# Kernel optimization log

Hardware: AMD Instinct MI355X
Metric: run time of the kernel (lower is better)

Reference implementation:

```python
import jax, jax.numpy as jnp
import numpy as np

N = 50000        # nodes
E = 800000       # directed edges (before self-loops)
F_IN = 128       # num_features
GAT_DIM = 16     # per-head channels
HEADS = 4
HID = GAT_DIM * HEADS   # 64, concat output of each GATConv
FC = 10 * GAT_DIM       # 160
OUT = 64                # output_dim
NEG_SLOPE = 0.2         # PyG GATConv default


def _gat_conv(x, W, a_src, a_dst, b, src, dst):
    """One PyG-style GATConv (concat=True, self-loops already in src/dst).
    x: [N, Fin], W: [Fin, HEADS*GAT_DIM], a_src/a_dst: [HEADS, GAT_DIM], b: [HEADS*GAT_DIM]."""
    H, C = a_src.shape
    h = (x @ W).reshape(N, H, C)                       # [N,H,C]
    s_src = (h * a_src).sum(-1)                        # [N,H] per-node src score
    s_dst = (h * a_dst).sum(-1)                        # [N,H]
    e = jax.nn.leaky_relu(s_src[src] + s_dst[dst], NEG_SLOPE)  # [Etot,H]
    # segment softmax over incoming edges of each destination node
    m = jax.ops.segment_max(e, dst, num_segments=N)    # [N,H]
    ex = jnp.exp(e - m[dst])
    z = jax.ops.segment_sum(ex, dst, num_segments=N)   # [N,H]
    alpha = ex / (z[dst] + 1e-16)                      # [Etot,H]
    msg = h[src] * alpha[:, :, None]                   # [Etot,H,C]
    out = jax.ops.segment_sum(msg, dst, num_segments=N)
    return out.reshape(N, H * C) + b


def setup_inputs() -> dict:
    key = jax.random.key(0)
    ks = jax.random.split(key, 20)
    sc = 0.05
    inp = {
        "x": jax.random.normal(ks[0], (N, F_IN), dtype=jnp.float32),
        "edge_index": jax.random.randint(ks[1], (2, E), 0, N, dtype=jnp.int32),
        "W0": jax.random.normal(ks[2], (F_IN, HID), dtype=jnp.float32) * sc,
        "as0": jax.random.normal(ks[3], (HEADS, GAT_DIM), dtype=jnp.float32) * sc,
        "ad0": jax.random.normal(ks[4], (HEADS, GAT_DIM), dtype=jnp.float32) * sc,
        "b0": jnp.zeros((HID,), jnp.float32),
        "W1": jax.random.normal(ks[5], (HID, HID), dtype=jnp.float32) * sc,
        "as1": jax.random.normal(ks[6], (HEADS, GAT_DIM), dtype=jnp.float32) * sc,
        "ad1": jax.random.normal(ks[7], (HEADS, GAT_DIM), dtype=jnp.float32) * sc,
        "b1": jnp.zeros((HID,), jnp.float32),
        "W2": jax.random.normal(ks[8], (HID, HID), dtype=jnp.float32) * sc,
        "as2": jax.random.normal(ks[9], (HEADS, GAT_DIM), dtype=jnp.float32) * sc,
        "ad2": jax.random.normal(ks[10], (HEADS, GAT_DIM), dtype=jnp.float32) * sc,
        "b2": jnp.zeros((HID,), jnp.float32),
        "fw1": jax.random.normal(ks[11], (HID, FC), dtype=jnp.float32) * sc,
        "fb1": jnp.zeros((FC,), jnp.float32),
        "fw2": jax.random.normal(ks[12], (FC, OUT), dtype=jnp.float32) * sc,
        "fb2": jnp.zeros((OUT,), jnp.float32),
    }
    return inp


def reference(x, edge_index, W0, as0, ad0, b0, W1, as1, ad1, b1, W2, as2, ad2, b2, fw1, fb1, fw2, fb2):
    loop = jnp.arange(N, dtype=edge_index.dtype)
    src = jnp.concatenate([edge_index[0], loop])   # PyG add_self_loops=True
    dst = jnp.concatenate([edge_index[1], loop])
    h = jax.nn.relu(_gat_conv(x, W0, as0, ad0, b0, src, dst))
    h = jax.nn.relu(_gat_conv(h, W1, as1, ad1, b1, src, dst))
    h = jax.nn.relu(_gat_conv(h, W2, as2, ad2, b2, src, dst))
    h = jax.nn.relu(h @ fw1 + fb1)
    return h @ fw2 + fb2
```

## Files before the change

### kernel.cpp

```cpp
#include <hip/hip_runtime.h>
#include <hip/hip_fp16.h>

#define NN 50000
#define EE 800000
#define ETOT (EE + NN)
#define HIDD 64
#define NHEADS 4
#define FCD 160
#define OUTD 64

#define NBKT 196
#define BSTRIDE 5120
#define CHUNK 4096
#define NEBLK ((ETOT + CHUNK - 1) / CHUNK)
#define NGB   ((NN + 63) / 64)
#define NFC128 ((NN + 127) / 128)


__global__ void k_zero(int* __restrict__ cursor) {
    int t = threadIdx.x;
    if (t < NBKT) cursor[t] = 0;
}

__global__ __launch_bounds__(256) void k_binwrite(const int* __restrict__ ei,
                                                  int* __restrict__ cursor,
                                                  unsigned* __restrict__ binned) {
    __shared__ int hist[NBKT];
    __shared__ int sbase[NBKT];
    __shared__ int cur[NBKT];
    int t = threadIdx.x;
    for (int i = t; i < NBKT; i += 256) hist[i] = 0;
    __syncthreads();
    int base = blockIdx.x * CHUNK;
    for (int k = t; k < CHUNK; k += 256) {
        int i = base + k;
        if (i < ETOT) {
            int dst = (i < EE) ? ei[EE + i] : (i - EE);
            atomicAdd(&hist[dst >> 8], 1);
        }
    }
    __syncthreads();
    for (int b = t; b < NBKT; b += 256) {
        int c = hist[b];
        sbase[b] = b * BSTRIDE + (c ? atomicAdd(&cursor[b], c) : 0);
        cur[b] = 0;
    }
    __syncthreads();
    for (int k = t; k < CHUNK; k += 256) {
        int i = base + k;
        if (i < ETOT) {
            int src, dst;
            if (i < EE) { src = ei[i]; dst = ei[EE + i]; }
            else { src = dst = i - EE; }
            int b = dst >> 8;
            int p = atomicAdd(&cur[b], 1);
            binned[sbase[b] + p] = ((unsigned)src << 8) | (unsigned)(dst & 255);
        }
    }
}

__global__ __launch_bounds__(256) void k_csr_final(const int* __restrict__ cursor,
                                                   const unsigned* __restrict__ binned,
                                                   int* __restrict__ rowbeg,
                                                   int* __restrict__ rowend,
                                                   int* __restrict__ csrc) {
    __shared__ int hist[256];
    __shared__ int cur[256];
    __shared__ int wsum[4];
    int b = blockIdx.x;
    int t = threadIdx.x;
    int s0 = b * BSTRIDE;
    int cnt = cursor[b];
    hist[t] = 0;
    __syncthreads();
    for (int k = t; k < cnt; k += 256) {
        unsigned pr = binned[s0 + k];
        atomicAdd(&hist[pr & 255u], 1);
    }
    __syncthreads();
    int v = hist[t];
    int lane = t & 63, w = t >> 6;
    int x = v;
    #pragma unroll
    for (int off = 1; off < 64; off <<= 1) {
        int y = __shfl_up(x, off);
        if (lane >= off) x += y;
    }
    if (lane == 63) wsum[w] = x;
    __syncthreads();
    int add = 0;
    #pragma unroll
    for (int k = 0; k < 4; k++) add += (k < w) ? wsum[k] : 0;
    int excl = x + add - v;
    int n = (b << 8) + t;
    if (n < NN) {
        rowbeg[n] = s0 + excl;
        rowend[n] = s0 + excl + v;
    }
    cur[t] = s0 + excl;
    __syncthreads();
    for (int k = t; k < cnt; k += 256) {
        unsigned pr = binned[s0 + k];
        int p = atomicAdd(&cur[pr & 255u], 1);
        csrc[p] = (int)(pr >> 8);
    }
}


template<int FIN>
__global__ __launch_bounds__(256) void k_gemm_scores(
        const float* __restrict__ x, const float* __restrict__ W,
        const float* __restrict__ a_src, const float* __restrict__ a_dst,
        __half* __restrict__ h, float* __restrict__ ssrc, float* __restrict__ sdst) {
    __shared__ float wl[64 * 64];
    __shared__ float xt[64][68];
    int t = threadIdx.x;
    int nb = blockIdx.x * 64;
    int qg = t & 15, ng = t >> 4;
    float acc[4][4] = {};
    const float4* wl4 = (const float4*)wl;

    #pragma unroll
    for (int p = 0; p < FIN / 64; p++) {
        if (p) __syncthreads();
        for (int i = t; i < 64 * 64 / 4; i += 256)
            ((float4*)wl)[i] = ((const float4*)W)[p * 1024 + i];
        #pragma unroll
        for (int r = 0; r < 4; r++) {
            int idx = t + r * 256;
            int node = idx & 63, kq = idx >> 6;
            int n = nb + node;
            float4 v = make_float4(0.f, 0.f, 0.f, 0.f);
            if (n < NN) v = *(const float4*)(x + (size_t)n * FIN + p * 64 + kq * 4);
            xt[kq * 4 + 0][node] = v.x;
            xt[kq * 4 + 1][node] = v.y;
            xt[kq * 4 + 2][node] = v.z;
            xt[kq * 4 + 3][node] = v.w;
        }
        __syncthreads();
        #pragma unroll 4
        for (int k = 0; k < 64; k++) {
            float4 wv = wl4[k * 16 + qg];
            float4 xv = *(const float4*)&xt[k][ng * 4];
            acc[0][0] += xv.x * wv.x; acc[0][1] += xv.x * wv.y;
            acc[0][2] += xv.x * wv.z; acc[0][3] += xv.x * wv.w;
            acc[1][0] += xv.y * wv.x; acc[1][1] += xv.y * wv.y;
            acc[1][2] += xv.y * wv.z; acc[1][3] += xv.y * wv.w;
            acc[2][0] += xv.z * wv.x; acc[2][1] += xv.z * wv.y;
            acc[2][2] += xv.z * wv.z; acc[2][3] += xv.z * wv.w;
            acc[3][0] += xv.w * wv.x; acc[3][1] += xv.w * wv.y;
            acc[3][2] += xv.w * wv.z; acc[3][3] += xv.w * wv.w;
        }
    }

    #pragma unroll
    for (int r = 0; r < 4; r++) {
        int n = nb + ng * 4 + r;
        if (n < NN) {
            union { __half2 h2[2]; uint2 u; } pk;
            pk.h2[0] = __floats2half2_rn(acc[r][0], acc[r][1]);
            pk.h2[1] = __floats2half2_rn(acc[r][2], acc[r][3]);
            *(uint2*)(h + (size_t)n * HIDD + qg * 4) = pk.u;
        }
    }

    float as0 = a_src[qg * 4 + 0], as1 = a_src[qg * 4 + 1];
    float as2 = a_src[qg * 4 + 2], as3 = a_src[qg * 4 + 3];
    float ad0 = a_dst[qg * 4 + 0], ad1 = a_dst[qg * 4 + 1];
    float ad2 = a_dst[qg * 4 + 2], ad3 = a_dst[qg * 4 + 3];
    float vs[4], vd[4];
    #pragma unroll
    for (int r = 0; r < 4; r++) {
        vs[r] = acc[r][0] * as0 + acc[r][1] * as1 + acc[r][2] * as2 + acc[r][3] * as3;
        vd[r] = acc[r][0] * ad0 + acc[r][1] * ad1 + acc[r][2] * ad2 + acc[r][3] * ad3;
        vs[r] += __shfl_xor(vs[r], 1); vs[r] += __shfl_xor(vs[r], 2);
        vd[r] += __shfl_xor(vd[r], 1); vd[r] += __shfl_xor(vd[r], 2);
    }
    if ((qg & 3) == 0) {
        int hd = qg >> 2;
        #pragma unroll
        for (int r = 0; r < 4; r++) {
            int n = nb + ng * 4 + r;
            if (n < NN) {
                ssrc[n * NHEADS + hd] = vs[r];
                sdst[n * NHEADS + hd] = vd[r];
            }
        }
    }
}


__global__ __launch_bounds__(512) void k_aggr_gemm(
        const __half* __restrict__ h, const float* __restrict__ ssrc,
        const float* __restrict__ sdst, const int* __restrict__ rowbeg,
        const int* __restrict__ rowend, const int* __restrict__ csrc,
        const float* __restrict__ bias, const float* __restrict__ W,
        const float* __restrict__ a_src, const float* __restrict__ a_dst,
        __half* __restrict__ hout, float* __restrict__ ssrc_o,
        float* __restrict__ sdst_o) {
    __shared__ float wl[64 * 64];
    __shared__ float xt[64][68];
    int t = threadIdx.x;
    int nb = blockIdx.x * 64;

    for (int i = t; i < 64 * 64 / 4; i += 512)
        ((float4*)wl)[i] = ((const float4*)W)[i];

    {
        int wid = t >> 6, lane = t & 63;
        int sub = lane >> 4, c4 = lane & 15, hd = c4 >> 2;
        #pragma unroll 1
        for (int i = 0; i < 8; i++) {
            int nl = wid * 8 + i;
            int n = nb + nl;
            float4 acc = make_float4(0.f, 0.f, 0.f, 0.f);
            float z = 0.f;
            if (n < NN) {
                int beg = rowbeg[n], end = rowend[n];
                float sdh = sdst[n * NHEADS + hd];
                for (int cb = beg; cb < end; cb += 16) {
                    #pragma unroll
                    for (int o = 0; o < 4; o++) {
                        int e = cb + sub + o * 4;
                        if (e < end) {
                            int s = csrc[e];
                            float eh = ssrc[s * NHEADS + hd] + sdh;
                            eh = eh > 0.f ? eh : 0.2f * eh;
                            float w = __expf(eh);
                            uint2 r = *(const uint2*)(h + (size_t)s * HIDD + c4 * 4);
                            float2 lo = __half22float2(*(__half2*)&r.x);
                            float2 hi = __half22float2(*(__half2*)&r.y);
                            acc.x += lo.x * w; acc.y += lo.y * w;
                            acc.z += hi.x * w; acc.w += hi.y * w;
                            z += w;
                        }
                    }
                }
            }
            acc.x += __shfl_xor(acc.x, 16); acc.y += __shfl_xor(acc.y, 16);
            acc.z += __shfl_xor(acc.z, 16); acc.w += __shfl_xor(acc.w, 16);
            z += __shfl_xor(z, 16);
            acc.x += __shfl_xor(acc.x, 32); acc.y += __shfl_xor(acc.y, 32);
            acc.z += __shfl_xor(acc.z, 32); acc.w += __shfl_xor(acc.w, 32);
            z += __shfl_xor(z, 32);
            if (sub == 0) {
                float inv_z = 1.0f / (z + 1e-16f);
                float4 bv = *(const float4*)(bias + c4 * 4);
                float v0 = acc.x * inv_z + bv.x; v0 = v0 > 0.f ? v0 : 0.f;
                float v1 = acc.y * inv_z + bv.y; v1 = v1 > 0.f ? v1 : 0.f;
                float v2 = acc.z * inv_z + bv.z; v2 = v2 > 0.f ? v2 : 0.f;
                float v3 = acc.w * inv_z + bv.w; v3 = v3 > 0.f ? v3 : 0.f;
                if (n >= NN) { v0 = v1 = v2 = v3 = 0.f; }
                xt[c4 * 4 + 0][nl] = v0;
                xt[c4 * 4 + 1][nl] = v1;
                xt[c4 * 4 + 2][nl] = v2;
                xt[c4 * 4 + 3][nl] = v3;
            }
        }
    }
    __syncthreads();

    {
        int qg = t & 15, ng = t >> 4;
        float acc[2][4] = {};
        const float4* wl4 = (const float4*)wl;
        #pragma unroll 4
        for (int k = 0; k < 64; k++) {
            float4 wv = wl4[k * 16 + qg];
            float2 xv = *(const float2*)&xt[k][ng * 2];
            acc[0][0] += xv.x * wv.x; acc[0][1] += xv.x * wv.y;
            acc[0][2] += xv.x * wv.z; acc[0][3] += xv.x * wv.w;
            acc[1][0] += xv.y * wv.x; acc[1][1] += xv.y * wv.y;
            acc[1][2] += xv.y * wv.z; acc[1][3] += xv.y * wv.w;
        }
        #pragma unroll
        for (int r = 0; r < 2; r++) {
            int n = nb + ng * 2 + r;
            if (n < NN) {
                union { __half2 h2[2]; uint2 u; } pk;
                pk.h2[0] = __floats2half2_rn(acc[r][0], acc[r][1]);
                pk.h2[1] = __floats2half2_rn(acc[r][2], acc[r][3]);
                *(uint2*)(hout + (size_t)n * HIDD + qg * 4) = pk.u;
            }
        }
        float as0 = a_src[qg * 4 + 0], as1 = a_src[qg * 4 + 1];
        float as2 = a_src[qg * 4 + 2], as3 = a_src[qg * 4 + 3];
        float ad0 = a_dst[qg * 4 + 0], ad1 = a_dst[qg * 4 + 1];
        float ad2 = a_dst[qg * 4 + 2], ad3 = a_dst[qg * 4 + 3];
        float vs[2], vd[2];
        #pragma unroll
        for (int r = 0; r < 2; r++) {
            vs[r] = acc[r][0] * as0 + acc[r][1] * as1 + acc[r][2] * as2 + acc[r][3] * as3;
            vd[r] = acc[r][0] * ad0 + acc[r][1] * ad1 + acc[r][2] * ad2 + acc[r][3] * ad3;
            vs[r] += __shfl_xor(vs[r], 1); vs[r] += __shfl_xor(vs[r], 2);
            vd[r] += __shfl_xor(vd[r], 1); vd[r] += __shfl_xor(vd[r], 2);
        }
        if ((qg & 3) == 0) {
            int hd = qg >> 2;
            #pragma unroll
            for (int r = 0; r < 2; r++) {
                int n = nb + ng * 2 + r;
                if (n < NN) {
                    ssrc_o[n * NHEADS + hd] = vs[r];
                    sdst_o[n * NHEADS + hd] = vd[r];
                }
            }
        }
    }
}


__global__ __launch_bounds__(256) void k_aggr(
        const __half* __restrict__ h, const float* __restrict__ ssrc,
        const float* __restrict__ sdst, const int* __restrict__ rowbeg,
        const int* __restrict__ rowend,
        const int* __restrict__ csrc, const float* __restrict__ bias,
        float* __restrict__ out) {
    int wid  = threadIdx.x >> 6;
    int lane = threadIdx.x & 63;
    int n = blockIdx.x * 4 + wid;
    int sub = lane >> 4;
    int c4  = lane & 15;
    int hd  = c4 >> 2;
    int beg = rowbeg[n], end = rowend[n];
    float sdh = sdst[n * NHEADS + hd];

    float4 acc = make_float4(0.f, 0.f, 0.f, 0.f);
    float z = 0.f;
    for (int cb = beg; cb < end; cb += 16) {
        #pragma unroll
        for (int o = 0; o < 4; o++) {
            int e = cb + sub + o * 4;
            if (e < end) {
                int s = csrc[e];
                float eh = ssrc[s * NHEADS + hd] + sdh;
                eh = eh > 0.f ? eh : 0.2f * eh;
                float w = __expf(eh);
                uint2 r = *(const uint2*)(h + (size_t)s * HIDD + c4 * 4);
                float2 lo = __half22float2(*(__half2*)&r.x);
                float2 hi = __half22float2(*(__half2*)&r.y);
                acc.x += lo.x * w; acc.y += lo.y * w;
                acc.z += hi.x * w; acc.w += hi.y * w;
                z += w;
            }
        }
    }
    acc.x += __shfl_xor(acc.x, 16); acc.y += __shfl_xor(acc.y, 16);
    acc.z += __shfl_xor(acc.z, 16); acc.w += __shfl_xor(acc.w, 16);
    z += __shfl_xor(z, 16);
    acc.x += __shfl_xor(acc.x, 32); acc.y += __shfl_xor(acc.y, 32);
    acc.z += __shfl_xor(acc.z, 32); acc.w += __shfl_xor(acc.w, 32);
    z += __shfl_xor(z, 32);

    if (sub == 0) {
        float inv_z = 1.0f / (z + 1e-16f);
        float4 bv = *(const float4*)(bias + c4 * 4);
        float4 o;
        o.x = acc.x * inv_z + bv.x; o.x = o.x > 0.f ? o.x : 0.f;
        o.y = acc.y * inv_z + bv.y; o.y = o.y > 0.f ? o.y : 0.f;
        o.z = acc.z * inv_z + bv.z; o.z = o.z > 0.f ? o.z : 0.f;
        o.w = acc.w * inv_z + bv.w; o.w = o.w > 0.f ? o.w : 0.f;
        *(float4*)(out + (size_t)n * HIDD + c4 * 4) = o;
    }
}


__global__ __launch_bounds__(256) void k_fc_fused(const float* __restrict__ x,
        const float* __restrict__ W1, const float* __restrict__ b1,
        const float* __restrict__ W2, const float* __restrict__ b2,
        float* __restrict__ out) {
    __shared__ float wl[32 * 160];
    __shared__ float xt[32][132];
    __shared__ __half y[160][136];
    int t = threadIdx.x;
    int nb = blockIdx.x * 128;
    const float4* wl4 = (const float4*)wl;

    {
        int qg = t & 7, ng = t >> 3;
        float acc[4][5][4] = {};
        #pragma unroll
        for (int p = 0; p < 2; p++) {
            if (p) __syncthreads();
            for (int i = t; i < 32 * 160 / 4; i += 256)
                ((float4*)wl)[i] = ((const float4*)W1)[p * 32 * 40 + i];
            #pragma unroll
            for (int r = 0; r < 4; r++) {
                int idx = t + r * 256;
                int node = idx & 127, kq = idx >> 7;
                int n = nb + node;
                float4 v = make_float4(0.f, 0.f, 0.f, 0.f);
                if (n < NN) v = *(const float4*)(x + (size_t)n * 64 + p * 32 + kq * 4);
                xt[kq * 4 + 0][node] = v.x;
                xt[kq * 4 + 1][node] = v.y;
                xt[kq * 4 + 2][node] = v.z;
                xt[kq * 4 + 3][node] = v.w;
            }
            __syncthreads();
            #pragma unroll 4
            for (int k = 0; k < 32; k++) {
                float4 xv = *(const float4*)&xt[k][ng * 4];
                #pragma unroll
                for (int i = 0; i < 5; i++) {
                    float4 wv = wl4[k * 40 + qg + 8 * i];
                    acc[0][i][0] += xv.x * wv.x; acc[0][i][1] += xv.x * wv.y;
                    acc[0][i][2] += xv.x * wv.z; acc[0][i][3] += xv.x * wv.w;
                    acc[1][i][0] += xv.y * wv.x; acc[1][i][1] += xv.y * wv.y;
                    acc[1][i][2] += xv.y * wv.z; acc[1][i][3] += xv.y * wv.w;
                    acc[2][i][0] += xv.z * wv.x; acc[2][i][1] += xv.z * wv.y;
                    acc[2][i][2] += xv.z * wv.z; acc[2][i][3] += xv.z * wv.w;
                    acc[3][i][0] += xv.w * wv.x; acc[3][i][1] += xv.w * wv.y;
                    acc[3][i][2] += xv.w * wv.z; acc[3][i][3] += xv.w * wv.w;
                }
            }
        }
        #pragma unroll
        for (int i = 0; i < 5; i++) {
            int j0 = (qg + 8 * i) * 4;
            float4 bv = *(const float4*)(b1 + j0);
            #pragma unroll
            for (int r = 0; r < 4; r++) {
                int node = ng * 4 + r;
                float v0 = acc[r][i][0] + bv.x; v0 = v0 > 0.f ? v0 : 0.f;
                float v1 = acc[r][i][1] + bv.y; v1 = v1 > 0.f ? v1 : 0.f;
                float v2 = acc[r][i][2] + bv.z; v2 = v2 > 0.f ? v2 : 0.f;
                float v3 = acc[r][i][3] + bv.w; v3 = v3 > 0.f ? v3 : 0.f;
                y[j0 + 0][node] = __float2half_rn(v0);
                y[j0 + 1][node] = __float2half_rn(v1);
                y[j0 + 2][node] = __float2half_rn(v2);
                y[j0 + 3][node] = __float2half_rn(v3);
            }
        }
    }
    __syncthreads();

    {
        int qg = t & 15, ng = t >> 4;
        float acc[8][4] = {};
        #pragma unroll
        for (int p = 0; p < 2; p++) {
            if (p) __syncthreads();
            for (int i = t; i < 80 * 64 / 4; i += 256)
                ((float4*)wl)[i] = ((const float4*)W2)[p * 80 * 16 + i];
            __syncthreads();
            #pragma unroll 2
            for (int k = 0; k < 80; k++) {
                float4 wv = wl4[k * 16 + qg];
                uint4 yr = *(const uint4*)&y[p * 80 + k][ng * 8];
                float2 f0 = __half22float2(*(__half2*)&yr.x);
                float2 f1 = __half22float2(*(__half2*)&yr.y);
                float2 f2 = __half22float2(*(__half2*)&yr.z);
                float2 f3 = __half22float2(*(__half2*)&yr.w);
                acc[0][0] += f0.x * wv.x; acc[0][1] += f0.x * wv.y;
                acc[0][2] += f0.x * wv.z; acc[0][3] += f0.x * wv.w;
                acc[1][0] += f0.y * wv.x; acc[1][1] += f0.y * wv.y;
                acc[1][2] += f0.y * wv.z; acc[1][3] += f0.y * wv.w;
                acc[2][0] += f1.x * wv.x; acc[2][1] += f1.x * wv.y;
                acc[2][2] += f1.x * wv.z; acc[2][3] += f1.x * wv.w;
                acc[3][0] += f1.y * wv.x; acc[3][1] += f1.y * wv.y;
                acc[3][2] += f1.y * wv.z; acc[3][3] += f1.y * wv.w;
                acc[4][0] += f2.x * wv.x; acc[4][1] += f2.x * wv.y;
                acc[4][2] += f2.x * wv.z; acc[4][3] += f2.x * wv.w;
                acc[5][0] += f2.y * wv.x; acc[5][1] += f2.y * wv.y;
                acc[5][2] += f2.y * wv.z; acc[5][3] += f2.y * wv.w;
                acc[6][0] += f3.x * wv.x; acc[6][1] += f3.x * wv.y;
                acc[6][2] += f3.x * wv.z; acc[6][3] += f3.x * wv.w;
                acc[7][0] += f3.y * wv.x; acc[7][1] += f3.y * wv.y;
                acc[7][2] += f3.y * wv.z; acc[7][3] += f3.y * wv.w;
            }
        }
        int j0 = qg * 4;
        float4 bv = *(const float4*)(b2 + j0);
        #pragma unroll
        for (int r = 0; r < 8; r++) {
            int n = nb + ng * 8 + r;
            if (n < NN) {
                float4 o;
                o.x = acc[r][0] + bv.x; o.y = acc[r][1] + bv.y;
                o.z = acc[r][2] + bv.z; o.w = acc[r][3] + bv.w;
                *(float4*)(out + (size_t)n * 64 + j0) = o;
            }
        }
    }
}


extern "C" void kernel_launch(void* const* d_in, const int* in_sizes, int n_in,
                              void* d_out, int out_size, void* d_ws, size_t ws_size,
                              hipStream_t stream) {
    const float* x   = (const float*)d_in[0];
    const int*   ei  = (const int*)d_in[1];
    const float* W0  = (const float*)d_in[2];
    const float* as0 = (const float*)d_in[3];
    const float* ad0 = (const float*)d_in[4];
    const float* b0  = (const float*)d_in[5];
    const float* W1  = (const float*)d_in[6];
    const float* as1 = (const float*)d_in[7];
    const float* ad1 = (const float*)d_in[8];
    const float* b1  = (const float*)d_in[9];
    const float* W2  = (const float*)d_in[10];
    const float* as2 = (const float*)d_in[11];
    const float* ad2 = (const float*)d_in[12];
    const float* b2  = (const float*)d_in[13];
    const float* fw1 = (const float*)d_in[14];
    const float* fb1 = (const float*)d_in[15];
    const float* fw2 = (const float*)d_in[16];
    const float* fb2 = (const float*)d_in[17];

    float* ws = (float*)d_ws;
    __half* hA  = (__half*)ws;
    __half* hB  = (__half*)(ws + (size_t)NN * 32);
    float* sAsrc = ws + (size_t)NN * 64;
    float* sAdst = sAsrc + (size_t)NN * NHEADS;
    float* sBsrc = sAdst + (size_t)NN * NHEADS;
    float* sBdst = sBsrc + (size_t)NN * NHEADS;
    float* act   = sBdst + (size_t)NN * NHEADS;
    float* scr   = act + (size_t)NN * HIDD;
    unsigned* binned = (unsigned*)scr;
    int*   csrc   = (int*)scr + 1100000;
    int*   rowbeg = (int*)scr + 2200000;
    int*   rowend = (int*)scr + 2300000;
    int*   cursor = (int*)scr + 2400000;

    k_zero<<<1, 256, 0, stream>>>(cursor);
    k_binwrite<<<NEBLK, 256, 0, stream>>>(ei, cursor, binned);
    k_csr_final<<<NBKT, 256, 0, stream>>>(cursor, binned, rowbeg, rowend, csrc);

    k_gemm_scores<128><<<NGB, 256, 0, stream>>>(x, W0, as0, ad0, hA, sAsrc, sAdst);
    k_aggr_gemm<<<NGB, 512, 0, stream>>>(hA, sAsrc, sAdst, rowbeg, rowend, csrc,
                                         b0, W1, as1, ad1, hB, sBsrc, sBdst);
    k_aggr_gemm<<<NGB, 512, 0, stream>>>(hB, sBsrc, sBdst, rowbeg, rowend, csrc,
                                         b1, W2, as2, ad2, hA, sAsrc, sAdst);
    k_aggr<<<NN / 4, 256, 0, stream>>>(hA, sAsrc, sAdst, rowbeg, rowend, csrc, b2, act);

    k_fc_fused<<<NFC128, 256, 0, stream>>>(act, fw1, fb1, fw2, fb2, (float*)d_out);
}
```

Before: 222.3 us.

## Fuse final GAT aggregation into the FC MLP kernel

```diff
diff --git a/kernel.cpp b/kernel.cpp
--- a/kernel.cpp
+++ b/kernel.cpp
@@ -310,96 +310,92 @@
 }
 
 
-__global__ __launch_bounds__(256) void k_aggr(
+__global__ __launch_bounds__(512) void k_aggr_fc(
         const __half* __restrict__ h, const float* __restrict__ ssrc,
         const float* __restrict__ sdst, const int* __restrict__ rowbeg,
-        const int* __restrict__ rowend,
-        const int* __restrict__ csrc, const float* __restrict__ bias,
-        float* __restrict__ out) {
-    int wid  = threadIdx.x >> 6;
-    int lane = threadIdx.x & 63;
-    int n = blockIdx.x * 4 + wid;
-    int sub = lane >> 4;
-    int c4  = lane & 15;
-    int hd  = c4 >> 2;
-    int beg = rowbeg[n], end = rowend[n];
-    float sdh = sdst[n * NHEADS + hd];
-
-    float4 acc = make_float4(0.f, 0.f, 0.f, 0.f);
-    float z = 0.f;
-    for (int cb = beg; cb < end; cb += 16) {
-        #pragma unroll
-        for (int o = 0; o < 4; o++) {
-            int e = cb + sub + o * 4;
-            if (e < end) {
-                int s = csrc[e];
-                float eh = ssrc[s * NHEADS + hd] + sdh;
-                eh = eh > 0.f ? eh : 0.2f * eh;
-                float w = __expf(eh);
-                uint2 r = *(const uint2*)(h + (size_t)s * HIDD + c4 * 4);
-                float2 lo = __half22float2(*(__half2*)&r.x);
-                float2 hi = __half22float2(*(__half2*)&r.y);
-                acc.x += lo.x * w; acc.y += lo.y * w;
-                acc.z += hi.x * w; acc.w += hi.y * w;
-                z += w;
-            }
-        }
-    }
-    acc.x += __shfl_xor(acc.x, 16); acc.y += __shfl_xor(acc.y, 16);
-    acc.z += __shfl_xor(acc.z, 16); acc.w += __shfl_xor(acc.w, 16);
-    z += __shfl_xor(z, 16);
-    acc.x += __shfl_xor(acc.x, 32); acc.y += __shfl_xor(acc.y, 32);
-    acc.z += __shfl_xor(acc.z, 32); acc.w += __shfl_xor(acc.w, 32);
-    z += __shfl_xor(z, 32);
-
-    if (sub == 0) {
-        float inv_z = 1.0f / (z + 1e-16f);
-        float4 bv = *(const float4*)(bias + c4 * 4);
-        float4 o;
-        o.x = acc.x * inv_z + bv.x; o.x = o.x > 0.f ? o.x : 0.f;
-        o.y = acc.y * inv_z + bv.y; o.y = o.y > 0.f ? o.y : 0.f;
-        o.z = acc.z * inv_z + bv.z; o.z = o.z > 0.f ? o.z : 0.f;
-        o.w = acc.w * inv_z + bv.w; o.w = o.w > 0.f ? o.w : 0.f;
-        *(float4*)(out + (size_t)n * HIDD + c4 * 4) = o;
-    }
-}
-
-
-__global__ __launch_bounds__(256) void k_fc_fused(const float* __restrict__ x,
+        const int* __restrict__ rowend, const int* __restrict__ csrc,
+        const float* __restrict__ bgat,
         const float* __restrict__ W1, const float* __restrict__ b1,
         const float* __restrict__ W2, const float* __restrict__ b2,
         float* __restrict__ out) {
     __shared__ float wl[32 * 160];
-    __shared__ float xt[32][132];
-    __shared__ __half y[160][136];
+    __shared__ __half xt[64][132];
+    __shared__ __half y[160][132];
     int t = threadIdx.x;
     int nb = blockIdx.x * 128;
     const float4* wl4 = (const float4*)wl;
 
+    for (int i = t; i < 32 * 160 / 4; i += 512)
+        ((float4*)wl)[i] = ((const float4*)W1)[i];
+
+    {
+        int wid = t >> 6, lane = t & 63;
+        int sub = lane >> 4, c4 = lane & 15, hd = c4 >> 2;
+        #pragma unroll 1
+        for (int i = 0; i < 16; i++) {
+            int nl = wid * 16 + i;
+            int n = nb + nl;
+            float4 acc = make_float4(0.f, 0.f, 0.f, 0.f);
+            float z = 0.f;
+            if (n < NN) {
+                int beg = rowbeg[n], end = rowend[n];
+                float sdh = sdst[n * NHEADS + hd];
+                for (int cb = beg; cb < end; cb += 16) {
+                    #pragma unroll
+                    for (int o = 0; o < 4; o++) {
+                        int e = cb + sub + o * 4;
+                        if (e < end) {
+                            int s = csrc[e];
+                            float eh = ssrc[s * NHEADS + hd] + sdh;
+                            eh = eh > 0.f ? eh : 0.2f * eh;
+                            float w = __expf(eh);
+                            uint2 r = *(const uint2*)(h + (size_t)s * HIDD + c4 * 4);
+                            float2 lo = __half22float2(*(__half2*)&r.x);
+                            float2 hi = __half22float2(*(__half2*)&r.y);
+                            acc.x += lo.x * w; acc.y += lo.y * w;
+                            acc.z += hi.x * w; acc.w += hi.y * w;
+                            z += w;
+                        }
+                    }
+                }
+            }
+            acc.x += __shfl_xor(acc.x, 16); acc.y += __shfl_xor(acc.y, 16);
+            acc.z += __shfl_xor(acc.z, 16); acc.w += __shfl_xor(acc.w, 16);
+            z += __shfl_xor(z, 16);
+            acc.x += __shfl_xor(acc.x, 32); acc.y += __shfl_xor(acc.y, 32);
+            acc.z += __shfl_xor(acc.z, 32); acc.w += __shfl_xor(acc.w, 32);
+            z += __shfl_xor(z, 32);
+            if (sub == 0) {
+                float inv_z = 1.0f / (z + 1e-16f);
+                float4 bv = *(const float4*)(bgat + c4 * 4);
+                float v0 = acc.x * inv_z + bv.x; v0 = v0 > 0.f ? v0 : 0.f;
+                float v1 = acc.y * inv_z + bv.y; v1 = v1 > 0.f ? v1 : 0.f;
+                float v2 = acc.z * inv_z + bv.z; v2 = v2 > 0.f ? v2 : 0.f;
+                float v3 = acc.w * inv_z + bv.w; v3 = v3 > 0.f ? v3 : 0.f;
+                if (n >= NN) { v0 = v1 = v2 = v3 = 0.f; }
+                xt[c4 * 4 + 0][nl] = __float2half_rn(v0);
+                xt[c4 * 4 + 1][nl] = __float2half_rn(v1);
+                xt[c4 * 4 + 2][nl] = __float2half_rn(v2);
+                xt[c4 * 4 + 3][nl] = __float2half_rn(v3);
+            }
+        }
+    }
+    __syncthreads();
+
     {
         int qg = t & 7, ng = t >> 3;
-        float acc[4][5][4] = {};
+        float acc[2][5][4] = {};
         #pragma unroll
         for (int p = 0; p < 2; p++) {
-            if (p) __syncthreads();
-            for (int i = t; i < 32 * 160 / 4; i += 256)
-                ((float4*)wl)[i] = ((const float4*)W1)[p * 32 * 40 + i];
-            #pragma unroll
-            for (int r = 0; r < 4; r++) {
-                int idx = t + r * 256;
-                int node = idx & 127, kq = idx >> 7;
-                int n = nb + node;
-                float4 v = make_float4(0.f, 0.f, 0.f, 0.f);
-                if (n < NN) v = *(const float4*)(x + (size_t)n * 64 + p * 32 + kq * 4);
-                xt[kq * 4 + 0][node] = v.x;
-                xt[kq * 4 + 1][node] = v.y;
-                xt[kq * 4 + 2][node] = v.z;
-                xt[kq * 4 + 3][node] = v.w;
-            }
-            __syncthreads();
+            if (p) {
+                __syncthreads();
+                for (int i = t; i < 32 * 160 / 4; i += 512)
+                    ((float4*)wl)[i] = ((const float4*)W1)[32 * 40 + i];
+                __syncthreads();
+            }
             #pragma unroll 4
             for (int k = 0; k < 32; k++) {
-                float4 xv = *(const float4*)&xt[k][ng * 4];
+                float2 xv = __half22float2(*(const __half2*)&xt[p * 32 + k][ng * 2]);
                 #pragma unroll
                 for (int i = 0; i < 5; i++) {
                     float4 wv = wl4[k * 40 + qg + 8 * i];
@@ -407,10 +403,6 @@
                     acc[0][i][2] += xv.x * wv.z; acc[0][i][3] += xv.x * wv.w;
                     acc[1][i][0] += xv.y * wv.x; acc[1][i][1] += xv.y * wv.y;
                     acc[1][i][2] += xv.y * wv.z; acc[1][i][3] += xv.y * wv.w;
-                    acc[2][i][0] += xv.z * wv.x; acc[2][i][1] += xv.z * wv.y;
-                    acc[2][i][2] += xv.z * wv.z; acc[2][i][3] += xv.z * wv.w;
-                    acc[3][i][0] += xv.w * wv.x; acc[3][i][1] += xv.w * wv.y;
-                    acc[3][i][2] += xv.w * wv.z; acc[3][i][3] += xv.w * wv.w;
                 }
             }
         }
@@ -419,8 +411,8 @@
             int j0 = (qg + 8 * i) * 4;
             float4 bv = *(const float4*)(b1 + j0);
             #pragma unroll
-            for (int r = 0; r < 4; r++) {
-                int node = ng * 4 + r;
+            for (int r = 0; r < 2; r++) {
+                int node = ng * 2 + r;
                 float v0 = acc[r][i][0] + bv.x; v0 = v0 > 0.f ? v0 : 0.f;
                 float v1 = acc[r][i][1] + bv.y; v1 = v1 > 0.f ? v1 : 0.f;
                 float v2 = acc[r][i][2] + bv.z; v2 = v2 > 0.f ? v2 : 0.f;
@@ -436,21 +428,19 @@
 
     {
         int qg = t & 15, ng = t >> 4;
-        float acc[8][4] = {};
+        float acc[4][4] = {};
         #pragma unroll
         for (int p = 0; p < 2; p++) {
             if (p) __syncthreads();
-            for (int i = t; i < 80 * 64 / 4; i += 256)
+            for (int i = t; i < 80 * 64 / 4; i += 512)
                 ((float4*)wl)[i] = ((const float4*)W2)[p * 80 * 16 + i];
             __syncthreads();
-            #pragma unroll 2
+            #pragma unroll 4
             for (int k = 0; k < 80; k++) {
                 float4 wv = wl4[k * 16 + qg];
-                uint4 yr = *(const uint4*)&y[p * 80 + k][ng * 8];
+                uint2 yr = *(const uint2*)&y[p * 80 + k][ng * 4];
                 float2 f0 = __half22float2(*(__half2*)&yr.x);
                 float2 f1 = __half22float2(*(__half2*)&yr.y);
-                float2 f2 = __half22float2(*(__half2*)&yr.z);
-                float2 f3 = __half22float2(*(__half2*)&yr.w);
                 acc[0][0] += f0.x * wv.x; acc[0][1] += f0.x * wv.y;
                 acc[0][2] += f0.x * wv.z; acc[0][3] += f0.x * wv.w;
                 acc[1][0] += f0.y * wv.x; acc[1][1] += f0.y * wv.y;
@@ -459,21 +449,13 @@
                 acc[2][2] += f1.x * wv.z; acc[2][3] += f1.x * wv.w;
                 acc[3][0] += f1.y * wv.x; acc[3][1] += f1.y * wv.y;
                 acc[3][2] += f1.y * wv.z; acc[3][3] += f1.y * wv.w;
-                acc[4][0] += f2.x * wv.x; acc[4][1] += f2.x * wv.y;
-                acc[4][2] += f2.x * wv.z; acc[4][3] += f2.x * wv.w;
-                acc[5][0] += f2.y * wv.x; acc[5][1] += f2.y * wv.y;
-                acc[5][2] += f2.y * wv.z; acc[5][3] += f2.y * wv.w;
-                acc[6][0] += f3.x * wv.x; acc[6][1] += f3.x * wv.y;
-                acc[6][2] += f3.x * wv.z; acc[6][3] += f3.x * wv.w;
-                acc[7][0] += f3.y * wv.x; acc[7][1] += f3.y * wv.y;
-                acc[7][2] += f3.y * wv.z; acc[7][3] += f3.y * wv.w;
             }
         }
         int j0 = qg * 4;
         float4 bv = *(const float4*)(b2 + j0);
         #pragma unroll
-        for (int r = 0; r < 8; r++) {
-            int n = nb + ng * 8 + r;
+        for (int r = 0; r < 4; r++) {
+            int n = nb + ng * 4 + r;
             if (n < NN) {
                 float4 o;
                 o.x = acc[r][0] + bv.x; o.y = acc[r][1] + bv.y;
@@ -514,8 +496,7 @@
     float* sAdst = sAsrc + (size_t)NN * NHEADS;
     float* sBsrc = sAdst + (size_t)NN * NHEADS;
     float* sBdst = sBsrc + (size_t)NN * NHEADS;
-    float* act   = sBdst + (size_t)NN * NHEADS;
-    float* scr   = act + (size_t)NN * HIDD;
+    float* scr   = sBdst + (size_t)NN * NHEADS;
     unsigned* binned = (unsigned*)scr;
     int*   csrc   = (int*)scr + 1100000;
     int*   rowbeg = (int*)scr + 2200000;
@@ -531,7 +512,6 @@
                                          b0, W1, as1, ad1, hB, sBsrc, sBdst);
     k_aggr_gemm<<<NGB, 512, 0, stream>>>(hB, sBsrc, sBdst, rowbeg, rowend, csrc,
                                          b1, W2, as2, ad2, hA, sAsrc, sAdst);
-    k_aggr<<<NN / 4, 256, 0, stream>>>(hA, sAsrc, sAdst, rowbeg, rowend, csrc, b2, act);
-
-    k_fc_fused<<<NFC128, 256, 0, stream>>>(act, fw1, fb1, fw2, fb2, (float*)d_out);
-}
+    k_aggr_fc<<<NFC128, 512, 0, stream>>>(hA, sAsrc, sAdst, rowbeg, rowend, csrc,
+                                          b2, fw1, fb1, fw2, fb2, (float*)d_out);
+}
```

After: 250.2 us. 1.13x slower.
